# Kernel tuning notes

Measured on AMD Instinct MI355X. Metric: run time of the kernel, lower is better.

The kernel has to match this reference:

```python
import jax, jax.numpy as jnp
import numpy as np

L = 2      # decoder layers
B = 4      # batch
T = 1000   # seq_len (mask built for this length)
C = 768    # input_dim / d_model
H = 12     # num_heads
DK = C // H
WIN = 100


def layernorm(x, g, b):
    m = x.mean(-1, keepdims=True)
    v = x.var(-1, keepdims=True)
    return (x - m) / jnp.sqrt(v + 1e-5) * g + b


def pos_encoding(t, c):
    # Transformer-XL / espnet RelPositionalEncoding table: relative positions t-1 .. -(t-1)
    rel = jnp.arange(t - 1, -t, -1, dtype=jnp.float32)          # (2t-1,)
    div = jnp.exp(-jnp.arange(0, c, 2, dtype=jnp.float32) * (np.log(10000.0) / c))
    ang = rel[:, None] * div[None, :]                            # (2t-1, c/2)
    pe = jnp.zeros((2 * t - 1, c), dtype=jnp.float32)
    pe = pe.at[:, 0::2].set(jnp.sin(ang)).at[:, 1::2].set(jnp.cos(ang))
    return pe


def rel_shift(x):
    # x: (B, H, T, 2T-1) -> (B, H, T, T), Transformer-XL relative shift
    b, h, t, p = x.shape
    xp = jnp.pad(x, ((0, 0), (0, 0), (0, 0), (1, 0)))
    xp = xp.reshape(b, h, p + 1, t)[:, :, 1:, :].reshape(b, h, t, p)
    return xp[..., :t]


def setup_inputs() -> dict:
    key = jax.random.key(0)
    ks = jax.random.split(key, 16)
    s = 0.02
    inp = {
        "x": jax.random.normal(ks[0], (B, T, C), dtype=jnp.float32),
        "Wq": jax.random.normal(ks[1], (L, C, C), dtype=jnp.float32) * s,
        "bq": jnp.zeros((L, C), dtype=jnp.float32),
        "Wk": jax.random.normal(ks[2], (L, C, C), dtype=jnp.float32) * s,
        "bk": jnp.zeros((L, C), dtype=jnp.float32),
        "Wv": jax.random.normal(ks[3], (L, C, C), dtype=jnp.float32) * s,
        "bv": jnp.zeros((L, C), dtype=jnp.float32),
        "Wo": jax.random.normal(ks[4], (L, C, C), dtype=jnp.float32) * s,
        "bo": jnp.zeros((L, C), dtype=jnp.float32),
        "Wp": jax.random.normal(ks[5], (L, C, C), dtype=jnp.float32) * s,   # linear_pos, no bias
        "pos_u": jax.random.normal(ks[6], (L, H, DK), dtype=jnp.float32) * s,
        "pos_v": jax.random.normal(ks[7], (L, H, DK), dtype=jnp.float32) * s,
        "ln1_g": jnp.ones((L, C), dtype=jnp.float32),
        "ln1_b": jnp.zeros((L, C), dtype=jnp.float32),
        "ln2_g": jnp.ones((L, C), dtype=jnp.float32),
        "ln2_b": jnp.zeros((L, C), dtype=jnp.float32),
        "W1": jax.random.normal(ks[8], (L, C, C), dtype=jnp.float32) * s,   # mlp_ratio = 1
        "b1": jnp.zeros((L, C), dtype=jnp.float32),
        "W2": jax.random.normal(ks[9], (L, C, C), dtype=jnp.float32) * s,
        "b2": jnp.zeros((L, C), dtype=jnp.float32),
    }
    # diagonal (banded) mask: True = blocked outside the attention window
    i = np.arange(T)
    blocked = np.abs(i[:, None] - i[None, :]) > (WIN // 2)
    inp["att_mask"] = jnp.asarray(blocked)
    return inp


def reference(x, att_mask, Wq, bq, Wk, bk, Wv, bv, Wo, bo, Wp, pos_u, pos_v,
              ln1_g, ln1_b, ln2_g, ln2_b, W1, b1, W2, b2):
    Bb, t, c = x.shape
    pe = pos_encoding(t, c)                       # (2T-1, C)
    h = x * jnp.sqrt(jnp.float32(c))              # xscale in RelPositionalEncoding
    for l in range(L):
        y = layernorm(h, ln1_g[l], ln1_b[l])
        q = (y @ Wq[l] + bq[l]).reshape(Bb, t, H, DK)
        k = (y @ Wk[l] + bk[l]).reshape(Bb, t, H, DK)
        v = (y @ Wv[l] + bv[l]).reshape(Bb, t, H, DK)
        p = (pe @ Wp[l]).reshape(2 * t - 1, H, DK)
        ac = jnp.einsum('bthd,bshd->bhts', q + pos_u[l], k)
        bd = rel_shift(jnp.einsum('bthd,phd->bhtp', q + pos_v[l], p))
        scores = (ac + bd) / jnp.sqrt(jnp.float32(DK))
        scores = jnp.where(att_mask[None, None], jnp.float32(-1e9), scores)
        attn = jax.nn.softmax(scores, axis=-1)
        o = jnp.einsum('bhts,bshd->bthd', attn, v).reshape(Bb, t, c)
        h = h + (o @ Wo[l] + bo[l])
        y2 = layernorm(h, ln2_g[l], ln2_b[l])
        h = h + (jax.nn.gelu(y2 @ W1[l] + b1[l]) @ W2[l] + b2[l])
    return h
```

## Files before the change

### kernel.cpp

```cpp
#include <hip/hip_runtime.h>
#include <math.h>

#define LNUM 2
#define BBATCH 4
#define TSEQ 1000
#define CDIM 768
#define HHEADS 12
#define DKK 64
#define PPOS (2*TSEQ-1)
#define HALFW 50
#define MROWS (BBATCH*TSEQ)
#define MPAD 4096
#define QKVDIM (3*CDIM)
#define NS 176

typedef __attribute__((ext_vector_type(8))) short s16x8;
typedef __attribute__((ext_vector_type(4))) short s16x4;
typedef __attribute__((ext_vector_type(4))) float f32x4;

#define LDSOFF(p) ((unsigned)(uintptr_t)(__attribute__((address_space(3))) const void*)(p))

__device__ __forceinline__ ushort f2bf(float x) {
    unsigned u = __float_as_uint(x);
    unsigned r = u + 0x7FFFu + ((u >> 16) & 1u);
    return (ushort)(r >> 16);
}
__device__ __forceinline__ float bf2f(ushort h) {
    return __uint_as_float(((unsigned)h) << 16);
}
__device__ __forceinline__ float gelu_f(float x) {
    float u = 0.7978845608028654f * (x + 0.044715f * x * x * x);
    return 0.5f * x * (1.f + tanhf(u));
}
__device__ __forceinline__ void gload_lds16(const void* g, void* l) {
    __builtin_amdgcn_global_load_lds(
        (const __attribute__((address_space(1))) void*)g,
        (__attribute__((address_space(3))) void*)l, 16, 0, 0);
}
__device__ __forceinline__ s16x4 tr_read(unsigned addr) {
    s16x4 d;
    asm volatile("ds_read_b64_tr_b16 %0, %1" : "=v"(d) : "v"(addr));
    return d;
}
__device__ __forceinline__ s16x4 tr_read128(unsigned addr) {
    s16x4 d;
    asm volatile("ds_read_b64_tr_b16 %0, %1 offset:128" : "=v"(d) : "v"(addr));
    return d;
}

__global__ __launch_bounds__(256) void transpose_pack(
    const float* __restrict__ Wq, const float* __restrict__ Wk,
    const float* __restrict__ Wv, const float* __restrict__ Wp,
    const float* __restrict__ Wo, const float* __restrict__ W1,
    const float* __restrict__ W2,
    ushort* __restrict__ Wtqkv, ushort* __restrict__ Wtp,
    ushort* __restrict__ Wto, ushort* __restrict__ Wt1, ushort* __restrict__ Wt2) {
    const int l = blockIdx.z / 7, m = blockIdx.z % 7;
    const float* srcs[7] = {Wq, Wk, Wv, Wp, Wo, W1, W2};
    const float* src = srcs[m] + (size_t)l * CDIM * CDIM;
    ushort* dst;
    if (m < 3)       dst = Wtqkv + (size_t)l * QKVDIM * CDIM + (size_t)m * CDIM * CDIM;
    else if (m == 3) dst = Wtp + (size_t)l * CDIM * CDIM;
    else if (m == 4) dst = Wto + (size_t)l * CDIM * CDIM;
    else if (m == 5) dst = Wt1 + (size_t)l * CDIM * CDIM;
    else             dst = Wt2 + (size_t)l * CDIM * CDIM;
    __shared__ float tile[32][33];
    const int tx = threadIdx.x, ty = threadIdx.y;
    const int c0 = blockIdx.x * 32, r0 = blockIdx.y * 32;
#pragma unroll
    for (int i = 0; i < 4; ++i)
        tile[ty + i * 8][tx] = src[(size_t)(r0 + ty + i * 8) * CDIM + c0 + tx];
    __syncthreads();
#pragma unroll
    for (int i = 0; i < 4; ++i)
        dst[(size_t)(c0 + ty + i * 8) * CDIM + r0 + tx] = f2bf(tile[tx][ty + i * 8]);
}

__global__ __launch_bounds__(256) void prep_small(ushort* __restrict__ pe,
                                                  const float* __restrict__ bq,
                                                  const float* __restrict__ bk,
                                                  const float* __restrict__ bv,
                                                  float* __restrict__ bqkv) {
    int idx = blockIdx.x * 256 + threadIdx.x;
    const int npair = 256 * (CDIM / 2);
    if (idx < npair) {
        int jloc = idx / (CDIM / 2);
        int m = idx - jloc * (CDIM / 2);
        int j = 896 + jloc;
        float rel = (float)(TSEQ - 1 - j);
        float div = expf(-(float)(2 * m) * (9.210340371976184f / (float)CDIM));
        float a = rel * div;
        pe[(size_t)j * CDIM + 2 * m]     = f2bf(sinf(a));
        pe[(size_t)j * CDIM + 2 * m + 1] = f2bf(cosf(a));
    }
    if (idx < LNUM * QKVDIM) {
        int l = idx / QKVDIM, c = idx - l * QKVDIM;
        float v;
        if (c < CDIM)            v = bq[l * CDIM + c];
        else if (c < 2 * CDIM)   v = bk[l * CDIM + c - CDIM];
        else                     v = bv[l * CDIM + c - 2 * CDIM];
        bqkv[idx] = v;
    }
}

__global__ __launch_bounds__(192) void ln_kernel(const float* __restrict__ in,
                                                 const float* __restrict__ g,
                                                 const float* __restrict__ bta,
                                                 ushort* __restrict__ y, float xscale) {
    const int row = blockIdx.x, tid = threadIdx.x;
    float4 v = *(const float4*)&in[(size_t)row * CDIM + tid * 4];
    v.x *= xscale; v.y *= xscale; v.z *= xscale; v.w *= xscale;
    float s  = v.x + v.y + v.z + v.w;
    float ss = v.x * v.x + v.y * v.y + v.z * v.z + v.w * v.w;
#pragma unroll
    for (int off = 32; off; off >>= 1) {
        s  += __shfl_xor(s, off);
        ss += __shfl_xor(ss, off);
    }
    __shared__ float sm[3], sq[3];
    const int wid = tid >> 6, lane = tid & 63;
    if (lane == 0) { sm[wid] = s; sq[wid] = ss; }
    __syncthreads();
    const float st  = sm[0] + sm[1] + sm[2];
    const float sst = sq[0] + sq[1] + sq[2];
    const float mean = st * (1.f / CDIM);
    const float var  = sst * (1.f / CDIM) - mean * mean;
    const float rstd = rsqrtf(var + 1e-5f);
    const float4 g4 = *(const float4*)&g[tid * 4];
    const float4 b4 = *(const float4*)&bta[tid * 4];
    ushort o0 = f2bf((v.x - mean) * rstd * g4.x + b4.x);
    ushort o1 = f2bf((v.y - mean) * rstd * g4.y + b4.y);
    ushort o2 = f2bf((v.z - mean) * rstd * g4.z + b4.z);
    ushort o3 = f2bf((v.w - mean) * rstd * g4.w + b4.w);
    uint2 pk; pk.x = (unsigned)o0 | ((unsigned)o1 << 16);
    pk.y = (unsigned)o2 | ((unsigned)o3 << 16);
    *(uint2*)&y[(size_t)row * CDIM + tid * 4] = pk;
}

template <int EPI>
__global__ __launch_bounds__(256, 3) void gemm64(const ushort* __restrict__ A,
                                                 const ushort* __restrict__ Bt,
                                                 const float* __restrict__ bias,
                                                 void* Out, int M, int ldo,
                                                 const float* resid, float rscale,
                                                 size_t zsB, size_t zsO) {
    __shared__ ushort lds[24576];
    const int tid = threadIdx.x;
    const int w = tid >> 6, lane = tid & 63;
    const int row0 = blockIdx.x * 64, col0 = blockIdx.y * 128;
    const size_t zb = blockIdx.z;
    Bt += zb * zsB;
    if (EPI == 2) Out = (void*)((float*)Out + zb * zsO);
    else          Out = (void*)((ushort*)Out + zb * zsO);

    const int srow8  = lane >> 3;
    const int schunk = (lane & 7) ^ srow8;

#define STAGE64(buf, k0)                                                        \
    {                                                                           \
        _Pragma("unroll")                                                       \
        for (int g = 0; g < 6; ++g) {                                           \
            const int grp = w * 6 + g;                                          \
            const int r = grp * 8 + srow8;                                      \
            const ushort* src = (grp < 8)                                       \
                ? A  + (size_t)(row0 + r) * CDIM + (k0) + schunk * 8            \
                : Bt + (size_t)(col0 + (r - 64)) * CDIM + (k0) + schunk * 8;    \
            gload_lds16(src, (char*)lds + (buf) * 24576 + grp * 1024);          \
        }                                                                       \
    }

    const int wm = (w >> 1) * 32, wn = (w & 1) * 64;
    const int lr = lane & 15, q = lane >> 4;
    f32x4 acc[2][4] = {};

    STAGE64(0, 0);
    __syncthreads();
    int cur = 0;
    for (int k0 = 0; k0 < CDIM; k0 += 64) {
        if (k0 + 64 < CDIM) STAGE64(cur ^ 1, k0 + 64);
        const int base = cur * 12288;
#pragma unroll
        for (int kk = 0; kk < 2; ++kk) {
            s16x8 af[2], bfr[4];
#pragma unroll
            for (int i = 0; i < 2; ++i) {
                const int r = wm + i * 16 + lr;
                af[i] = *(const s16x8*)&lds[base + r * 64 + ((((kk << 2) | q) ^ (r & 7)) << 3)];
            }
#pragma unroll
            for (int j = 0; j < 4; ++j) {
                const int r = 64 + wn + j * 16 + lr;
                bfr[j] = *(const s16x8*)&lds[base + r * 64 + ((((kk << 2) | q) ^ (r & 7)) << 3)];
            }
#pragma unroll
            for (int i = 0; i < 2; ++i)
#pragma unroll
                for (int j = 0; j < 4; ++j)
                    acc[i][j] = __builtin_amdgcn_mfma_f32_16x16x32_bf16(af[i], bfr[j], acc[i][j], 0, 0, 0);
        }
        __syncthreads();
        cur ^= 1;
    }
#undef STAGE64

    const int lrr = (lane >> 4) * 4;
    const int lc = lane & 15;
#pragma unroll
    for (int j = 0; j < 4; ++j) {
        const int col = col0 + wn + j * 16 + lc;
        const float bv = bias ? bias[col] : 0.f;
#pragma unroll
        for (int i = 0; i < 2; ++i) {
#pragma unroll
            for (int r = 0; r < 4; ++r) {
                const int row = row0 + wm + i * 16 + lrr + r;
                if (row >= M) continue;
                const float v = acc[i][j][r] + bv;
                if (EPI == 0)
                    ((ushort*)Out)[(size_t)row * ldo + col] = f2bf(v);
                else if (EPI == 1)
                    ((ushort*)Out)[(size_t)row * ldo + col] = f2bf(gelu_f(v));
                else {
                    float* p = (float*)Out + (size_t)row * ldo + col;
                    *p = resid[(size_t)row * ldo + col] * rscale + v;
                }
            }
        }
    }
}

__global__ __launch_bounds__(256, 3) void attn_mfma(
    const ushort* __restrict__ qkv, const ushort* __restrict__ pb,
    const float* __restrict__ pos_u, const float* __restrict__ pos_v,
    ushort* __restrict__ o) {
    __shared__ __align__(16) char smem[51200];
    ushort* Kl   = (ushort*)smem;
    ushort* Pl   = (ushort*)smem;
    ushort* Vsub = (ushort*)(smem + 25600);
    ushort* Bd   = (ushort*)(smem + 37888);

    const int tid = threadIdx.x;
    const int w = tid >> 6, lane = tid & 63;
    const int t0 = blockIdx.x * 64;
    const int h = blockIdx.y, b = blockIdx.z;
    const int m0 = w * 16;
    const int lr = lane & 15, lk = (lane >> 4) * 8, q = lane >> 4;

    auto vsrc = [&](int sp) -> const ushort* {
        const int ob = sp * 1024 + lane * 16;
        const int d0c = ob / 6144;
        const int rem = ob - d0c * 6144;
        const int j = rem >> 5;
        const int halfo = (rem & 31) >> 4;
        int t = t0 - HALFW + j; t = t < 0 ? 0 : (t < TSEQ ? t : TSEQ - 1);
        return qkv + (size_t)(b * TSEQ + t) * QKVDIM + 2 * CDIM + h * DKK
               + (d0c & 1) * 16 + halfo * 8;
    };

    int tq = t0 + m0 + lr; tq = tq < TSEQ ? tq : TSEQ - 1;
    const ushort* qp = qkv + (size_t)(b * TSEQ + tq) * QKVDIM + h * DKK;
    s16x8 qr0 = *(const s16x8*)(qp + lk);
    s16x8 qr1 = *(const s16x8*)(qp + 32 + lk);
    const float* puB = pos_u + h * DKK;
    const float* pvB = pos_v + h * DKK;
    float puA[16], pvA[16];
    *(float4*)&puA[0]  = *(const float4*)(puB + lk);
    *(float4*)&puA[4]  = *(const float4*)(puB + lk + 4);
    *(float4*)&puA[8]  = *(const float4*)(puB + 32 + lk);
    *(float4*)&puA[12] = *(const float4*)(puB + 32 + lk + 4);
    *(float4*)&pvA[0]  = *(const float4*)(pvB + lk);
    *(float4*)&pvA[4]  = *(const float4*)(pvB + lk + 4);
    *(float4*)&pvA[8]  = *(const float4*)(pvB + 32 + lk);
    *(float4*)&pvA[12] = *(const float4*)(pvB + 32 + lk + 4);

    const ushort* pbh = pb + (size_t)949 * CDIM + h * DKK;
    s16x8 pfr[7][2];
#pragma unroll
    for (int uf = 0; uf < 7; ++uf) {
        pfr[uf][0] = *(const s16x8*)&pbh[(size_t)(uf * 16 + lr) * CDIM + lk];
        pfr[uf][1] = *(const s16x8*)&pbh[(size_t)(uf * 16 + lr) * CDIM + 32 + lk];
    }

#pragma unroll
    for (int g = 0; g < 3; ++g) {
        const int sp = w * 3 + g;
        gload_lds16(vsrc(sp), (char*)Vsub + sp * 1024);
    }

    {
        const int srow8 = lane >> 3;
        const int schunk = (lane & 7) ^ srow8;
#pragma unroll
        for (int g = 0; g < 6; ++g) {
            const int sp = w * 6 + g;
            if (sp < 22) {
                const int r = sp * 8 + srow8;
                int kb = t0 - HALFW + r; kb = kb < 0 ? 0 : (kb < TSEQ ? kb : TSEQ - 1);
                const ushort* src = qkv + (size_t)(b * TSEQ + kb) * QKVDIM + CDIM
                                    + h * DKK + schunk * 8;
                gload_lds16(src, (char*)Kl + sp * 1024);
            }
        }
    }

    s16x8 qu0, qu1, qv0, qv1;
#pragma unroll
    for (int e = 0; e < 8; ++e) {
        const float q0 = bf2f((ushort)qr0[e]), q1 = bf2f((ushort)qr1[e]);
        qu0[e] = (short)f2bf(q0 + puA[e]);
        qu1[e] = (short)f2bf(q1 + puA[8 + e]);
        qv0[e] = (short)f2bf(q0 + pvA[e]);
        qv1[e] = (short)f2bf(q1 + pvA[8 + e]);
    }
    __syncthreads();

    const f32x4 zero = {0.f, 0.f, 0.f, 0.f};
    f32x4 acS[11], acB[7];
    __builtin_amdgcn_s_setprio(1);
#pragma unroll
    for (int uf = 0; uf < 7; ++uf) {
        acB[uf] = __builtin_amdgcn_mfma_f32_16x16x32_bf16(qv0, pfr[uf][0], zero, 0, 0, 0);
        acB[uf] = __builtin_amdgcn_mfma_f32_16x16x32_bf16(qv1, pfr[uf][1], acB[uf], 0, 0, 0);
    }
#pragma unroll
    for (int jf = 0; jf < 11; ++jf) {
        const int rr = jf * 16 + lr;
        const int sw = rr & 7;
        s16x8 k0 = *(const s16x8*)&Kl[rr * 64 + (((q)     ^ sw) << 3)];
        s16x8 k1 = *(const s16x8*)&Kl[rr * 64 + (((q | 4) ^ sw) << 3)];
        acS[jf] = __builtin_amdgcn_mfma_f32_16x16x32_bf16(qu0, k0, zero, 0, 0, 0);
        acS[jf] = __builtin_amdgcn_mfma_f32_16x16x32_bf16(qu1, k1, acS[jf], 0, 0, 0);
    }
    __builtin_amdgcn_s_setprio(0);

    ushort* bdw = Bd + w * 16 * 104;
#pragma unroll
    for (int uf = 0; uf < 7; ++uf)
#pragma unroll
        for (int r = 0; r < 4; ++r)
            bdw[((lane >> 4) * 4 + r) * 104 + uf * 16 + lr] = f2bf(acB[uf][r]);
    float mx[4] = {-1e30f, -1e30f, -1e30f, -1e30f};
#pragma unroll
    for (int jf = 0; jf < 11; ++jf)
#pragma unroll
        for (int r = 0; r < 4; ++r) {
            const int tl = (lane >> 4) * 4 + r;
            const int tloc = m0 + tl;
            const int j = jf * 16 + lr;
            const int u = j - tloc;
            const int s = t0 - HALFW + j;
            const bool valid = (u >= 0) & (u <= 2 * HALFW) & (s >= 0) & (s < TSEQ)
                               & (t0 + tloc < TSEQ);
            float sc = -1e30f;
            if (valid) sc = (acS[jf][r] + bf2f(bdw[tl * 104 + u])) * 0.125f;
            acS[jf][r] = sc;
            mx[r] = fmaxf(mx[r], sc);
        }
#pragma unroll
    for (int r = 0; r < 4; ++r)
#pragma unroll
        for (int off = 8; off; off >>= 1)
            mx[r] = fmaxf(mx[r], __shfl_xor(mx[r], off));
    float sm[4] = {0.f, 0.f, 0.f, 0.f};
#pragma unroll
    for (int jf = 0; jf < 11; ++jf)
#pragma unroll
        for (int r = 0; r < 4; ++r) {
            float e = __expf(acS[jf][r] - mx[r]);
            acS[jf][r] = e;
            sm[r] += e;
        }
#pragma unroll
    for (int r = 0; r < 4; ++r) {
#pragma unroll
        for (int off = 8; off; off >>= 1) sm[r] += __shfl_xor(sm[r], off);
        sm[r] = 1.f / sm[r];
    }
    __syncthreads();

    s16x8 vr0 = *vsrc(12 + w * 3 + 0);
    s16x8 vr1 = *vsrc(12 + w * 3 + 1);
    s16x8 vr2 = *vsrc(12 + w * 3 + 2);

#pragma unroll
    for (int jf = 0; jf < 11; ++jf)
#pragma unroll
        for (int r = 0; r < 4; ++r)
            Pl[(m0 + (lane >> 4) * 4 + r) * 200 + jf * 16 + lr] = f2bf(acS[jf][r]);
#pragma unroll
    for (int r = 0; r < 4; ++r)
        Pl[(m0 + (lane >> 4) * 4 + r) * 200 + 176 + lr] = 0;

    s16x8 pa[6];
#pragma unroll
    for (int ks = 0; ks < 6; ++ks)
        pa[ks] = *(const s16x8*)&Pl[(m0 + lr) * 200 + ks * 32 + lk];

    const unsigned vbase = LDSOFF(Vsub);
#pragma unroll
    for (int nf = 0; nf < 2; ++nf) {
        const unsigned abase = vbase + (nf & 1) * 6144 + ((lane >> 4) << 8) + ((lane & 15) << 1);
        s16x4 lo[6], hi[6];
#pragma unroll
        for (int ks = 0; ks < 6; ++ks) {
            lo[ks] = tr_read(abase + ks * 1024);
            hi[ks] = tr_read128(abase + ks * 1024);
        }
        asm volatile("s_waitcnt lgkmcnt(0)" ::: "memory");
        __builtin_amdgcn_sched_barrier(0);
        f32x4 acO = {};
        __builtin_amdgcn_s_setprio(1);
#pragma unroll
        for (int ks = 0; ks < 6; ++ks) {
            s16x8 vb = __builtin_shufflevector(lo[ks], hi[ks], 0, 1, 2, 3, 4, 5, 6, 7);
            acO = __builtin_amdgcn_mfma_f32_16x16x32_bf16(pa[ks], vb, acO, 0, 0, 0);
        }
        __builtin_amdgcn_s_setprio(0);
#pragma unroll
        for (int r = 0; r < 4; ++r) {
            const int t = t0 + m0 + (lane >> 4) * 4 + r;
            if (t < TSEQ)
                o[(size_t)(b * TSEQ + t) * CDIM + h * DKK + nf * 16 + lr] =
                    f2bf(acO[r] * sm[r]);
        }
    }
    __syncthreads();

    *(s16x8*)((char*)Vsub + (w * 3 + 0) * 1024 + lane * 16) = vr0;
    *(s16x8*)((char*)Vsub + (w * 3 + 1) * 1024 + lane * 16) = vr1;
    *(s16x8*)((char*)Vsub + (w * 3 + 2) * 1024 + lane * 16) = vr2;
    __syncthreads();

#pragma unroll
    for (int nf = 2; nf < 4; ++nf) {
        const unsigned abase = vbase + (nf & 1) * 6144 + ((lane >> 4) << 8) + ((lane & 15) << 1);
        s16x4 lo[6], hi[6];
#pragma unroll
        for (int ks = 0; ks < 6; ++ks) {
            lo[ks] = tr_read(abase + ks * 1024);
            hi[ks] = tr_read128(abase + ks * 1024);
        }
        asm volatile("s_waitcnt lgkmcnt(0)" ::: "memory");
        __builtin_amdgcn_sched_barrier(0);
        f32x4 acO = {};
        __builtin_amdgcn_s_setprio(1);
#pragma unroll
        for (int ks = 0; ks < 6; ++ks) {
            s16x8 vb = __builtin_shufflevector(lo[ks], hi[ks], 0, 1, 2, 3, 4, 5, 6, 7);
            acO = __builtin_amdgcn_mfma_f32_16x16x32_bf16(pa[ks], vb, acO, 0, 0, 0);
        }
        __builtin_amdgcn_s_setprio(0);
#pragma unroll
        for (int r = 0; r < 4; ++r) {
            const int t = t0 + m0 + (lane >> 4) * 4 + r;
            if (t < TSEQ)
                o[(size_t)(b * TSEQ + t) * CDIM + h * DKK + nf * 16 + lr] =
                    f2bf(acO[r] * sm[r]);
        }
    }
}

extern "C" void kernel_launch(void* const* d_in, const int* in_sizes, int n_in,
                              void* d_out, int out_size, void* d_ws, size_t ws_size,
                              hipStream_t stream) {
    const float* x     = (const float*)d_in[0];
    const float* Wq    = (const float*)d_in[1];
    const float* bq    = (const float*)d_in[2];
    const float* Wk    = (const float*)d_in[3];
    const float* bk    = (const float*)d_in[4];
    const float* Wv    = (const float*)d_in[5];
    const float* bv    = (const float*)d_in[6];
    const float* Wo    = (const float*)d_in[7];
    const float* bo    = (const float*)d_in[8];
    const float* Wp    = (const float*)d_in[9];
    const float* pos_u = (const float*)d_in[10];
    const float* pos_v = (const float*)d_in[11];
    const float* ln1g  = (const float*)d_in[12];
    const float* ln1b  = (const float*)d_in[13];
    const float* ln2g  = (const float*)d_in[14];
    const float* ln2b  = (const float*)d_in[15];
    const float* W1    = (const float*)d_in[16];
    const float* b1    = (const float*)d_in[17];
    const float* W2    = (const float*)d_in[18];
    const float* b2    = (const float*)d_in[19];

    float* h = (float*)d_out;
    const float XS = 27.712812921102035f;

    char* p = (char*)d_ws;
    ushort* Wtqkv = (ushort*)p;               p += (size_t)LNUM * QKVDIM * CDIM * 2;
    ushort* Wtp   = (ushort*)p;               p += (size_t)LNUM * CDIM * CDIM * 2;
    ushort* Wto   = (ushort*)p;               p += (size_t)LNUM * CDIM * CDIM * 2;
    ushort* Wt1   = (ushort*)p;               p += (size_t)LNUM * CDIM * CDIM * 2;
    ushort* Wt2   = (ushort*)p;               p += (size_t)LNUM * CDIM * CDIM * 2;
    float*  bqkv  = (float*)p;                p += (size_t)LNUM * QKVDIM * 4;
    ushort* pe    = (ushort*)p;               p += (size_t)2048 * CDIM * 2;
    ushort* pb    = (ushort*)p;               p += (size_t)LNUM * 2048 * CDIM * 2;
    ushort* y     = (ushort*)p;               p += (size_t)MPAD * CDIM * 2;
    ushort* qkv   = (ushort*)p;               p += (size_t)MPAD * QKVDIM * 2;
    ushort* o     = (ushort*)p;               p += (size_t)MPAD * CDIM * 2;
    ushort* hid   = (ushort*)p;               p += (size_t)MPAD * CDIM * 2;

    transpose_pack<<<dim3(24, 24, LNUM * 7), dim3(32, 8), 0, stream>>>(
        Wq, Wk, Wv, Wp, Wo, W1, W2, Wtqkv, Wtp, Wto, Wt1, Wt2);
    prep_small<<<384, 256, 0, stream>>>(pe, bq, bk, bv, bqkv);

    const int MB = (MROWS + 63) / 64;
    const dim3 gQKV(MB, QKVDIM / 128);
    const dim3 gC(MB, CDIM / 128);
    const dim3 gP(4, CDIM / 128, LNUM);
    const dim3 gA(16, HHEADS, BBATCH);

    gemm64<0><<<gP, 256, 0, stream>>>(pe + (size_t)896 * CDIM, Wtp, nullptr,
                                      pb + (size_t)896 * CDIM, 256, CDIM,
                                      nullptr, 0.f,
                                      (size_t)CDIM * CDIM, (size_t)2048 * CDIM);

    for (int l = 0; l < LNUM; ++l) {
        const size_t wo = (size_t)l * CDIM * CDIM;
        const float* res1 = (l == 0) ? x : h;
        const float rs1   = (l == 0) ? XS : 1.f;
        ln_kernel<<<MROWS, 192, 0, stream>>>(res1, ln1g + l * CDIM, ln1b + l * CDIM, y, rs1);
        gemm64<0><<<gQKV, 256, 0, stream>>>(y, Wtqkv + (size_t)l * QKVDIM * CDIM,
                                            bqkv + l * QKVDIM, qkv, MROWS, QKVDIM,
                                            nullptr, 0.f, 0, 0);
        attn_mfma<<<gA, 256, 0, stream>>>(
            qkv, pb + (size_t)l * 2048 * CDIM,
            pos_u + l * HHEADS * DKK, pos_v + l * HHEADS * DKK, o);
        gemm64<2><<<gC, 256, 0, stream>>>(o, Wto + wo, bo + l * CDIM, h, MROWS, CDIM,
                                          res1, rs1, 0, 0);
        ln_kernel<<<MROWS, 192, 0, stream>>>(h, ln2g + l * CDIM, ln2b + l * CDIM, y, 1.f);
        gemm64<1><<<gC, 256, 0, stream>>>(y, Wt1 + wo, b1 + l * CDIM, hid, MROWS, CDIM,
                                          nullptr, 0.f, 0, 0);
        gemm64<2><<<gC, 256, 0, stream>>>(hid, Wt2 + wo, b2 + l * CDIM, h, MROWS, CDIM,
                                          h, 1.f, 0, 0);
    }
}
```

Baseline: 261.5 us.

## Convert tiled GEMM into persistent work-stealing kernel with atomic tile counter

Replaces the grid-indexed GEMM with a persistent kernel. A fixed number of blocks repeatedly claims 64x128 output tiles from a global atomic counter until all tiles are taken. The counters are zeroed with a memset at the start of each call, and each GEMM launch uses its own counter. The positional-projection GEMM is now launched once per layer rather than batched over the z dimension. The aim is to cut block launch and scheduling overhead and balance tail work, at the cost of an atomic plus a barrier per tile and some lost occupancy flexibility.

```diff
diff --git a/kernel.cpp b/kernel.cpp
--- a/kernel.cpp
+++ b/kernel.cpp
@@ -138,23 +138,28 @@
 }
 
 template <int EPI>
-__global__ __launch_bounds__(256, 3) void gemm64(const ushort* __restrict__ A,
-                                                 const ushort* __restrict__ Bt,
-                                                 const float* __restrict__ bias,
-                                                 void* Out, int M, int ldo,
-                                                 const float* resid, float rscale,
-                                                 size_t zsB, size_t zsO) {
+__global__ __launch_bounds__(256, 3) void gemm_ws(const ushort* __restrict__ A,
+                                                  const ushort* __restrict__ Bt,
+                                                  const float* __restrict__ bias,
+                                                  void* Out, int M, int ldo,
+                                                  const float* resid, float rscale,
+                                                  unsigned* ctr, int nrow, int ntiles) {
     __shared__ ushort lds[24576];
+    __shared__ int stile;
     const int tid = threadIdx.x;
     const int w = tid >> 6, lane = tid & 63;
-    const int row0 = blockIdx.x * 64, col0 = blockIdx.y * 128;
-    const size_t zb = blockIdx.z;
-    Bt += zb * zsB;
-    if (EPI == 2) Out = (void*)((float*)Out + zb * zsO);
-    else          Out = (void*)((ushort*)Out + zb * zsO);
-
     const int srow8  = lane >> 3;
     const int schunk = (lane & 7) ^ srow8;
+    const int wm = (w >> 1) * 32, wn = (w & 1) * 64;
+    const int lr = lane & 15, q = lane >> 4;
+
+    for (;;) {
+        if (tid == 0) stile = (int)atomicAdd(ctr, 1u);
+        __syncthreads();
+        const int t = stile;
+        if (t >= ntiles) break;
+        const int row0 = (t % nrow) * 64;
+        const int col0 = (t / nrow) * 128;
 
 #define STAGE64(buf, k0)                                                        \
     {                                                                           \
@@ -169,60 +174,58 @@
         }                                                                       \
     }
 
-    const int wm = (w >> 1) * 32, wn = (w & 1) * 64;
-    const int lr = lane & 15, q = lane >> 4;
-    f32x4 acc[2][4] = {};
-
-    STAGE64(0, 0);
-    __syncthreads();
-    int cur = 0;
-    for (int k0 = 0; k0 < CDIM; k0 += 64) {
-        if (k0 + 64 < CDIM) STAGE64(cur ^ 1, k0 + 64);
-        const int base = cur * 12288;
-#pragma unroll
-        for (int kk = 0; kk < 2; ++kk) {
-            s16x8 af[2], bfr[4];
+        f32x4 acc[2][4] = {};
+        STAGE64(0, 0);
+        __syncthreads();
+        int cur = 0;
+        for (int k0 = 0; k0 < CDIM; k0 += 64) {
+            if (k0 + 64 < CDIM) STAGE64(cur ^ 1, k0 + 64);
+            const int base = cur * 12288;
+#pragma unroll
+            for (int kk = 0; kk < 2; ++kk) {
+                s16x8 af[2], bfr[4];
+#pragma unroll
+                for (int i = 0; i < 2; ++i) {
+                    const int r = wm + i * 16 + lr;
+                    af[i] = *(const s16x8*)&lds[base + r * 64 + ((((kk << 2) | q) ^ (r & 7)) << 3)];
+                }
+#pragma unroll
+                for (int j = 0; j < 4; ++j) {
+                    const int r = 64 + wn + j * 16 + lr;
+                    bfr[j] = *(const s16x8*)&lds[base + r * 64 + ((((kk << 2) | q) ^ (r & 7)) << 3)];
+                }
+#pragma unroll
+                for (int i = 0; i < 2; ++i)
+#pragma unroll
+                    for (int j = 0; j < 4; ++j)
+                        acc[i][j] = __builtin_amdgcn_mfma_f32_16x16x32_bf16(af[i], bfr[j], acc[i][j], 0, 0, 0);
+            }
+            __syncthreads();
+            cur ^= 1;
+        }
+#undef STAGE64
+
+        const int lrr = (lane >> 4) * 4;
+        const int lc = lane & 15;
+#pragma unroll
+        for (int j = 0; j < 4; ++j) {
+            const int col = col0 + wn + j * 16 + lc;
+            const float bv = bias ? bias[col] : 0.f;
 #pragma unroll
             for (int i = 0; i < 2; ++i) {
-                const int r = wm + i * 16 + lr;
-                af[i] = *(const s16x8*)&lds[base + r * 64 + ((((kk << 2) | q) ^ (r & 7)) << 3)];
-            }
-#pragma unroll
-            for (int j = 0; j < 4; ++j) {
-                const int r = 64 + wn + j * 16 + lr;
-                bfr[j] = *(const s16x8*)&lds[base + r * 64 + ((((kk << 2) | q) ^ (r & 7)) << 3)];
-            }
-#pragma unroll
-            for (int i = 0; i < 2; ++i)
-#pragma unroll
-                for (int j = 0; j < 4; ++j)
-                    acc[i][j] = __builtin_amdgcn_mfma_f32_16x16x32_bf16(af[i], bfr[j], acc[i][j], 0, 0, 0);
-        }
-        __syncthreads();
-        cur ^= 1;
-    }
-#undef STAGE64
-
-    const int lrr = (lane >> 4) * 4;
-    const int lc = lane & 15;
-#pragma unroll
-    for (int j = 0; j < 4; ++j) {
-        const int col = col0 + wn + j * 16 + lc;
-        const float bv = bias ? bias[col] : 0.f;
-#pragma unroll
-        for (int i = 0; i < 2; ++i) {
-#pragma unroll
-            for (int r = 0; r < 4; ++r) {
-                const int row = row0 + wm + i * 16 + lrr + r;
-                if (row >= M) continue;
-                const float v = acc[i][j][r] + bv;
-                if (EPI == 0)
-                    ((ushort*)Out)[(size_t)row * ldo + col] = f2bf(v);
-                else if (EPI == 1)
-                    ((ushort*)Out)[(size_t)row * ldo + col] = f2bf(gelu_f(v));
-                else {
-                    float* p = (float*)Out + (size_t)row * ldo + col;
-                    *p = resid[(size_t)row * ldo + col] * rscale + v;
+#pragma unroll
+                for (int r = 0; r < 4; ++r) {
+                    const int row = row0 + wm + i * 16 + lrr + r;
+                    if (row >= M) continue;
+                    const float v = acc[i][j][r] + bv;
+                    if (EPI == 0)
+                        ((ushort*)Out)[(size_t)row * ldo + col] = f2bf(v);
+                    else if (EPI == 1)
+                        ((ushort*)Out)[(size_t)row * ldo + col] = f2bf(gelu_f(v));
+                    else {
+                        float* p = (float*)Out + (size_t)row * ldo + col;
+                        *p = resid[(size_t)row * ldo + col] * rscale + v;
+                    }
                 }
             }
         }
@@ -500,39 +503,41 @@
     ushort* qkv   = (ushort*)p;               p += (size_t)MPAD * QKVDIM * 2;
     ushort* o     = (ushort*)p;               p += (size_t)MPAD * CDIM * 2;
     ushort* hid   = (ushort*)p;               p += (size_t)MPAD * CDIM * 2;
-
+    unsigned* ctr = (unsigned*)p;             p += 16 * sizeof(unsigned);
+
+    hipMemsetAsync(ctr, 0, 16 * sizeof(unsigned), stream);
     transpose_pack<<<dim3(24, 24, LNUM * 7), dim3(32, 8), 0, stream>>>(
         Wq, Wk, Wv, Wp, Wo, W1, W2, Wtqkv, Wtp, Wto, Wt1, Wt2);
     prep_small<<<384, 256, 0, stream>>>(pe, bq, bk, bv, bqkv);
 
     const int MB = (MROWS + 63) / 64;
-    const dim3 gQKV(MB, QKVDIM / 128);
-    const dim3 gC(MB, CDIM / 128);
-    const dim3 gP(4, CDIM / 128, LNUM);
+    const int GW = 768;
     const dim3 gA(16, HHEADS, BBATCH);
-
-    gemm64<0><<<gP, 256, 0, stream>>>(pe + (size_t)896 * CDIM, Wtp, nullptr,
-                                      pb + (size_t)896 * CDIM, 256, CDIM,
-                                      nullptr, 0.f,
-                                      (size_t)CDIM * CDIM, (size_t)2048 * CDIM);
+    int ci = 0;
+
+    for (int l = 0; l < LNUM; ++l)
+        gemm_ws<0><<<24, 256, 0, stream>>>(pe + (size_t)896 * CDIM,
+                                           Wtp + (size_t)l * CDIM * CDIM, nullptr,
+                                           pb + (size_t)l * 2048 * CDIM + (size_t)896 * CDIM,
+                                           256, CDIM, nullptr, 0.f, ctr + ci++, 4, 24);
 
     for (int l = 0; l < LNUM; ++l) {
         const size_t wo = (size_t)l * CDIM * CDIM;
         const float* res1 = (l == 0) ? x : h;
         const float rs1   = (l == 0) ? XS : 1.f;
         ln_kernel<<<MROWS, 192, 0, stream>>>(res1, ln1g + l * CDIM, ln1b + l * CDIM, y, rs1);
-        gemm64<0><<<gQKV, 256, 0, stream>>>(y, Wtqkv + (size_t)l * QKVDIM * CDIM,
-                                            bqkv + l * QKVDIM, qkv, MROWS, QKVDIM,
-                                            nullptr, 0.f, 0, 0);
+        gemm_ws<0><<<GW, 256, 0, stream>>>(y, Wtqkv + (size_t)l * QKVDIM * CDIM,
+                                           bqkv + l * QKVDIM, qkv, MROWS, QKVDIM,
+                                           nullptr, 0.f, ctr + ci++, MB, MB * (QKVDIM / 128));
         attn_mfma<<<gA, 256, 0, stream>>>(
             qkv, pb + (size_t)l * 2048 * CDIM,
             pos_u + l * HHEADS * DKK, pos_v + l * HHEADS * DKK, o);
-        gemm64<2><<<gC, 256, 0, stream>>>(o, Wto + wo, bo + l * CDIM, h, MROWS, CDIM,
-                                          res1, rs1, 0, 0);
+        gemm_ws<2><<<GW, 256, 0, stream>>>(o, Wto + wo, bo + l * CDIM, h, MROWS, CDIM,
+                                           res1, rs1, ctr + ci++, MB, MB * (CDIM / 128));
         ln_kernel<<<MROWS, 192, 0, stream>>>(h, ln2g + l * CDIM, ln2b + l * CDIM, y, 1.f);
-        gemm64<1><<<gC, 256, 0, stream>>>(y, Wt1 + wo, b1 + l * CDIM, hid, MROWS, CDIM,
-                                          nullptr, 0.f, 0, 0);
-        gemm64<2><<<gC, 256, 0, stream>>>(hid, Wt2 + wo, b2 + l * CDIM, h, MROWS, CDIM,
-                                          h, 1.f, 0, 0);
-    }
-}
+        gemm_ws<1><<<GW, 256, 0, stream>>>(y, Wt1 + wo, b1 + l * CDIM, hid, MROWS, CDIM,
+                                           nullptr, 0.f, ctr + ci++, MB, MB * (CDIM / 128));
+        gemm_ws<2><<<GW, 256, 0, stream>>>(hid, Wt2 + wo, b2 + l * CDIM, h, MROWS, CDIM,
+                                           h, 1.f, ctr + ci++, MB, MB * (CDIM / 128));
+    }
+}
```

Measured after the change: 366.7 us. +40.2%, slower.
